# Performance work log

Measured on AMD Instinct MI355X. Metric: run time of the kernel, lower is better.

Reference implementation:

```python
import jax, jax.numpy as jnp
import numpy as np

B, T, D = 2, 2048, 1024
HEADS = 16
MEM = 512
HEAD_DIM = D // HEADS


def setup_inputs() -> dict:
    key = jax.random.key(0)
    k1, k2, k3, k4, k5 = jax.random.split(key, 5)
    x = jax.random.normal(k1, (B, T, D), dtype=jnp.float32)
    w_qkv = jax.random.normal(k2, (3 * D, D), dtype=jnp.float32) * (1.0 / np.sqrt(D))
    w_out = jax.random.normal(k3, (D, D), dtype=jnp.float32) * (1.0 / np.sqrt(D))
    b_out = jax.random.normal(k4, (D,), dtype=jnp.float32) * 0.01
    memory = jax.random.normal(k5, (MEM, D), dtype=jnp.float32)
    return {"x": x, "w_qkv": w_qkv, "w_out": w_out, "b_out": b_out, "memory": memory}


def reference(x, w_qkv, w_out, b_out, memory):
    b, t, d = x.shape
    h, hd = HEADS, HEAD_DIM
    scale = hd ** -0.5
    # QKV projection: [B,T,3D]
    qkv = jnp.einsum('btd,ed->bte', x, w_qkv)
    q, k, v = jnp.split(qkv, 3, axis=-1)
    # [B,H,T,hd]
    q = q.reshape(b, t, h, hd).transpose(0, 2, 1, 3)
    k = k.reshape(b, t, h, hd).transpose(0, 2, 1, 3)
    v = v.reshape(b, t, h, hd).transpose(0, 2, 1, 3)
    # memory K/V: [B,H,MEM,hd] (broadcast over batch)
    mem = memory.reshape(1, MEM, h, hd).transpose(0, 2, 1, 3)
    mem = jnp.broadcast_to(mem, (b, h, MEM, hd))
    k = jnp.concatenate([mem, k], axis=2)
    v = jnp.concatenate([mem, v], axis=2)
    # attention: scores [B,H,T,MEM+T]
    scores = jnp.einsum('bhqd,bhkd->bhqk', q, k) * scale
    weights = jax.nn.softmax(scores, axis=-1)
    out = jnp.einsum('bhqk,bhkd->bhqd', weights, v)
    out = out.transpose(0, 2, 1, 3).reshape(b, t, d)
    return jnp.einsum('btd,ed->bte', out, w_out) + b_out
```

## Files before the change

### kernel.cpp

```cpp
#include <hip/hip_runtime.h>
#include <hip/hip_bf16.h>
#include <stdint.h>

#define B_   2
#define T_   2048
#define D_   1024
#define H_   16
#define HD_  64
#define MEM_ 512
#define KV_  (MEM_ + T_)
#define NIT_ (KV_ / 64)

using bf16 = __bf16;
typedef __bf16 bf16x8 __attribute__((ext_vector_type(8)));
typedef float  f32x4  __attribute__((ext_vector_type(4)));
typedef short  s16x4  __attribute__((ext_vector_type(4)));

__device__ __forceinline__ f32x4 mfma16(bf16x8 a, bf16x8 b, f32x4 c) {
  return __builtin_amdgcn_mfma_f32_16x16x32_bf16(a, b, c, 0, 0, 0);
}
__device__ __forceinline__ f32x4 mfma16k16(s16x4 a, s16x4 b, f32x4 c) {
  return __builtin_amdgcn_mfma_f32_16x16x16bf16_1k(a, b, c, 0, 0, 0);
}

template <bool F32>
__device__ __forceinline__ bf16x8 load8(const void* p, size_t off) {
  if constexpr (F32) {
    const float* q = (const float*)p + off;
    f32x4 u = *(const f32x4*)q;
    f32x4 v = *(const f32x4*)(q + 4);
    bf16x8 r;
    r[0] = (bf16)u[0]; r[1] = (bf16)u[1]; r[2] = (bf16)u[2]; r[3] = (bf16)u[3];
    r[4] = (bf16)v[0]; r[5] = (bf16)v[1]; r[6] = (bf16)v[2]; r[7] = (bf16)v[3];
    return r;
  } else {
    return *(const bf16x8*)((const bf16*)p + off);
  }
}

__device__ __forceinline__ unsigned short bf16_bits(float f) {
  bf16 h = (bf16)f;
  return __builtin_bit_cast(unsigned short, h);
}

__device__ __forceinline__ ushort4 pack4(f32x4 v) {
  ushort4 p;
  p.x = bf16_bits(v[0]); p.y = bf16_bits(v[1]);
  p.z = bf16_bits(v[2]); p.w = bf16_bits(v[3]);
  return p;
}

__global__ void fill_mem(const float* __restrict__ memory,
                         bf16* __restrict__ mem_k, bf16* __restrict__ mem_vt) {
  int idx = blockIdx.x * 256 + threadIdx.x;
  int m = idx >> 10, d = idx & 1023;
  bf16 v = (bf16)memory[idx];
  mem_k[idx] = v;
  mem_vt[(size_t)d * MEM_ + m] = v;
}

template <int EPI, bool AF32, bool WF32, bool APLANE>
__global__ __launch_bounds__(256) void gemm_bt(
    const void* __restrict__ A, const void* __restrict__ W,
    const float* __restrict__ bias,
    bf16* __restrict__ q_ws, bf16* __restrict__ k_ws, bf16* __restrict__ vt_ws,
    float* __restrict__ Cout, int K) {
  __shared__ __align__(16) bf16 Als[128 * 32];
  __shared__ __align__(16) bf16 Bls[128 * 32];
  const int m0 = blockIdx.y * 128;
  const int n0 = blockIdx.x * 128;
  const int tid = threadIdx.x;
  const int w = tid >> 6;
  const int lane = tid & 63;
  const int lx = lane & 15;
  const int quad = lane >> 4;
  const int amb = (w & 1) * 64;
  const int bnb = (w >> 1) * 64;
  const int r0 = tid >> 2, seg = tid & 3;

  f32x4 acc[4][4];
#pragma unroll
  for (int i = 0; i < 4; i++)
#pragma unroll
    for (int j = 0; j < 4; j++) acc[i][j] = (f32x4){0.f, 0.f, 0.f, 0.f};

  for (int k0 = 0; k0 < K; k0 += 32) {
    bf16x8 a0, a1;
    if constexpr (APLANE) {
      int c0 = k0 + seg * 8, h = c0 >> 6, hd = c0 & 63;
      int mA = m0 + r0, mB = m0 + 64 + r0;
      a0 = load8<false>(A,
          ((size_t)((mA >> 11) * H_ + h) * T_ + (mA & 2047)) * HD_ + hd);
      a1 = load8<false>(A,
          ((size_t)((mB >> 11) * H_ + h) * T_ + (mB & 2047)) * HD_ + hd);
    } else {
      a0 = load8<AF32>(A, (size_t)(m0 + r0) * K + k0 + seg * 8);
      a1 = load8<AF32>(A, (size_t)(m0 + 64 + r0) * K + k0 + seg * 8);
    }
    bf16x8 b0 = load8<WF32>(W, (size_t)(n0 + r0) * K + k0 + seg * 8);
    bf16x8 b1 = load8<WF32>(W, (size_t)(n0 + 64 + r0) * K + k0 + seg * 8);
    __syncthreads();
    *(bf16x8*)&Als[tid * 8] = a0;
    *(bf16x8*)&Als[2048 + tid * 8] = a1;
    *(bf16x8*)&Bls[tid * 8] = b0;
    *(bf16x8*)&Bls[2048 + tid * 8] = b1;
    __syncthreads();

    bf16x8 af[4], bfr[4];
#pragma unroll
    for (int mt = 0; mt < 4; mt++)
      af[mt] = *(const bf16x8*)&Als[(amb + mt * 16 + lx) * 32 + quad * 8];
#pragma unroll
    for (int nt = 0; nt < 4; nt++)
      bfr[nt] = *(const bf16x8*)&Bls[(bnb + nt * 16 + lx) * 32 + quad * 8];
#pragma unroll
    for (int mt = 0; mt < 4; mt++)
#pragma unroll
      for (int nt = 0; nt < 4; nt++)
        acc[mt][nt] = mfma16(af[mt], bfr[nt], acc[mt][nt]);
  }

  if (EPI == 0) {
#pragma unroll
    for (int mt = 0; mt < 4; mt++) {
      int mbase = m0 + amb + mt * 16 + quad * 4;
      int b = mbase >> 11;
      int t = mbase & 2047;
#pragma unroll
      for (int nt = 0; nt < 4; nt++) {
        int col = n0 + bnb + nt * 16 + lx;
        int which = col >> 10;
        int d = col & 1023;
        int h = d >> 6, hdi = d & 63;
        int bh = b * H_ + h;
        if (which == 0) {
#pragma unroll
          for (int r = 0; r < 4; r++)
            q_ws[((size_t)bh * T_ + t + r) * HD_ + hdi] = (bf16)acc[mt][nt][r];
        } else if (which == 1) {
#pragma unroll
          for (int r = 0; r < 4; r++)
            k_ws[((size_t)bh * T_ + t + r) * HD_ + hdi] = (bf16)acc[mt][nt][r];
        } else {
          *(ushort4*)&vt_ws[((size_t)bh * HD_ + hdi) * T_ + t] =
              pack4(acc[mt][nt]);
        }
      }
    }
  } else {
#pragma unroll
    for (int nt = 0; nt < 4; nt++) {
      int col = n0 + bnb + nt * 16 + lx;
      float bias_f = bias[col];
#pragma unroll
      for (int mt = 0; mt < 4; mt++) {
        int mbase = m0 + amb + mt * 16 + quad * 4;
#pragma unroll
        for (int r = 0; r < 4; r++)
          Cout[(size_t)(mbase + r) * D_ + col] = acc[mt][nt][r] + bias_f;
      }
    }
  }
}

__global__ __launch_bounds__(256, 2) void attn_kernel(
    bf16* __restrict__ q_ws, const bf16* __restrict__ k_ws,
    const bf16* __restrict__ vt_ws, const bf16* __restrict__ mem_k,
    const bf16* __restrict__ mem_vt) {
  __shared__ __align__(16) bf16 Kls[64][72];
  __shared__ __align__(16) bf16 Vls[64][72];
  const int tid = threadIdx.x;
  const int w = tid >> 6;
  const int lane = tid & 63;
  const int lx = lane & 15;
  const int quad = lane >> 4;
  const int bh = blockIdx.x & 31;
  const int qt = blockIdx.x >> 5;
  const int q0 = qt * 128 + w * 32;
  const int h = bh & 15;

  const int srow1 = tid >> 3, soff1 = (tid & 7) * 8;
  const int srow2 = (tid + 256) >> 3, soff2 = soff1;

  bf16* qbase = q_ws + ((size_t)bh * T_ + q0) * HD_;

  const float QSCALE = 0.125f * 1.44269504089f;
  bf16x8 qf[2][2];
#pragma unroll
  for (int qg = 0; qg < 2; qg++)
#pragma unroll
    for (int hf = 0; hf < 2; hf++) {
      bf16x8 v = *(const bf16x8*)(qbase + (size_t)(qg * 16 + lx) * HD_ +
                                  hf * 32 + quad * 8);
#pragma unroll
      for (int i = 0; i < 8; i++)
        v[i] = (bf16)((float)v[i] * QSCALE);
      qf[qg][hf] = v;
    }

  const bf16* kplane = k_ws + (size_t)bh * T_ * HD_;
  const bf16* vtplane = vt_ws + (size_t)bh * HD_ * T_;
  const bf16* mkh = mem_k + h * HD_;
  const bf16* mvh = mem_vt + (size_t)h * HD_ * MEM_;

  f32x4 o[4][2];
#pragma unroll
  for (int mt = 0; mt < 4; mt++)
#pragma unroll
    for (int qg = 0; qg < 2; qg++) o[mt][qg] = (f32x4){0.f, 0.f, 0.f, 0.f};
  float lsum[2] = {0.f, 0.f};

  for (int it = 0; it < NIT_; it++) {
    const int kv0 = it * 64;
    const bool memPart = kv0 < MEM_;
    bf16x8 kr1, kr2, vr1, vr2;
    if (memPart) {
      kr1 = *(const bf16x8*)(mkh + (size_t)(kv0 + srow1) * D_ + soff1);
      kr2 = *(const bf16x8*)(mkh + (size_t)(kv0 + srow2) * D_ + soff2);
      vr1 = *(const bf16x8*)(mvh + (size_t)srow1 * MEM_ + kv0 + soff1);
      vr2 = *(const bf16x8*)(mvh + (size_t)srow2 * MEM_ + kv0 + soff2);
    } else {
      const int t0 = kv0 - MEM_;
      kr1 = *(const bf16x8*)(kplane + (size_t)(t0 + srow1) * HD_ + soff1);
      kr2 = *(const bf16x8*)(kplane + (size_t)(t0 + srow2) * HD_ + soff2);
      vr1 = *(const bf16x8*)(vtplane + (size_t)srow1 * T_ + t0 + soff1);
      vr2 = *(const bf16x8*)(vtplane + (size_t)srow2 * T_ + t0 + soff2);
    }
    __syncthreads();
    *(bf16x8*)&Kls[srow1][soff1] = kr1;
    *(bf16x8*)&Kls[srow2][soff2] = kr2;
    *(bf16x8*)&Vls[srow1][soff1] = vr1;
    *(bf16x8*)&Vls[srow2][soff2] = vr2;
    __syncthreads();

    f32x4 s[4][2];
#pragma unroll
    for (int g = 0; g < 4; g++) {
      bf16x8 ka0 = *(const bf16x8*)&Kls[g * 16 + lx][quad * 8];
      bf16x8 ka1 = *(const bf16x8*)&Kls[g * 16 + lx][32 + quad * 8];
#pragma unroll
      for (int qg = 0; qg < 2; qg++) {
        s[g][qg] = (f32x4){0.f, 0.f, 0.f, 0.f};
        s[g][qg] = mfma16(ka0, qf[qg][0], s[g][qg]);
        s[g][qg] = mfma16(ka1, qf[qg][1], s[g][qg]);
      }
    }

    s16x4 pb[2][4];
#pragma unroll
    for (int qg = 0; qg < 2; qg++) {
      float ps = 0.f;
#pragma unroll
      for (int g = 0; g < 4; g++) {
#pragma unroll
        for (int r = 0; r < 4; r++) {
          float p = __builtin_amdgcn_exp2f(s[g][qg][r]);
          ps += p;
          pb[qg][g][r] = (short)bf16_bits(p);
        }
      }
      lsum[qg] += ps;
    }

#pragma unroll
    for (int mt = 0; mt < 4; mt++) {
#pragma unroll
      for (int kk = 0; kk < 4; kk++) {
        s16x4 va = *(const s16x4*)&Vls[mt * 16 + lx][kk * 16 + quad * 4];
#pragma unroll
        for (int qg = 0; qg < 2; qg++)
          o[mt][qg] = mfma16k16(va, pb[qg][kk], o[mt][qg]);
      }
    }
  }

  float inv[2];
#pragma unroll
  for (int qg = 0; qg < 2; qg++) {
    float s2 = lsum[qg];
    s2 += __shfl_xor(s2, 16);
    s2 += __shfl_xor(s2, 32);
    inv[qg] = 1.f / s2;
  }

#pragma unroll
  for (int qg = 0; qg < 2; qg++) {
#pragma unroll
    for (int mt = 0; mt < 4; mt++) {
      f32x4 ov;
#pragma unroll
      for (int r = 0; r < 4; r++) ov[r] = o[mt][qg][r] * inv[qg];
      *(ushort4*)(qbase + (size_t)(qg * 16 + lx) * HD_ + mt * 16 + quad * 4)
          = pack4(ov);
    }
  }
}

extern "C" void kernel_launch(void* const* d_in, const int* in_sizes, int n_in,
                              void* d_out, int out_size, void* d_ws,
                              size_t ws_size, hipStream_t stream) {
  const void*  x      = d_in[0];
  const void*  w_qkv  = d_in[1];
  const void*  w_out  = d_in[2];
  const float* b_out  = (const float*)d_in[3];
  const float* memory = (const float*)d_in[4];

  char* ws = (char*)d_ws;
  bf16* q_ws   = (bf16*)(ws);
  bf16* k_ws   = (bf16*)(ws + (8u << 20));
  bf16* vt_ws  = (bf16*)(ws + (16u << 20));
  bf16* mem_k  = (bf16*)(ws + (24u << 20));
  bf16* mem_vt = (bf16*)(ws + (25u << 20));
  float* out = (float*)d_out;

  fill_mem<<<dim3(2048), dim3(256), 0, stream>>>(memory, mem_k, mem_vt);
  gemm_bt<0, true, true, false><<<dim3(24, 32), dim3(256), 0, stream>>>(
      x, w_qkv, nullptr, q_ws, k_ws, vt_ws, nullptr, 1024);
  attn_kernel<<<dim3(512), dim3(256), 0, stream>>>(
      q_ws, k_ws, vt_ws, mem_k, mem_vt);
  gemm_bt<1, false, true, true><<<dim3(8, 32), dim3(256), 0, stream>>>(
      q_ws, w_out, b_out, nullptr, nullptr, nullptr, out, 1024);
}
```

Measured before the change: 222.9 us.

## Fuse memory fill into QKV GEMM and double attention KV tile

Removes the separate fill_mem launch by adding an extra row of blocks to the QKV GEMM grid that converts memory to bf16 K and transposed V, reading with vectorised float4 loads. The attention kernel now stages 128 KV rows per iteration instead of 64, processing them in two halves, which halves the number of barrier pairs and global-load rounds. This costs more LDS per block, which may reduce occupancy. The fill blocks also run alongside GEMM blocks and keep scattered transposed stores.

```diff
diff --git a/kernel.cpp b/kernel.cpp
--- a/kernel.cpp
+++ b/kernel.cpp
@@ -9,7 +9,7 @@
 #define HD_  64
 #define MEM_ 512
 #define KV_  (MEM_ + T_)
-#define NIT_ (KV_ / 64)
+#define NIT2_ (KV_ / 128)
 
 using bf16 = __bf16;
 typedef __bf16 bf16x8 __attribute__((ext_vector_type(8)));
@@ -50,26 +50,35 @@
   return p;
 }
 
-__global__ void fill_mem(const float* __restrict__ memory,
-                         bf16* __restrict__ mem_k, bf16* __restrict__ mem_vt) {
-  int idx = blockIdx.x * 256 + threadIdx.x;
-  int m = idx >> 10, d = idx & 1023;
-  bf16 v = (bf16)memory[idx];
-  mem_k[idx] = v;
-  mem_vt[(size_t)d * MEM_ + m] = v;
-}
-
-template <int EPI, bool AF32, bool WF32, bool APLANE>
+template <int EPI, bool AF32, bool WF32, bool APLANE, bool FUSEFILL>
 __global__ __launch_bounds__(256) void gemm_bt(
     const void* __restrict__ A, const void* __restrict__ W,
     const float* __restrict__ bias,
     bf16* __restrict__ q_ws, bf16* __restrict__ k_ws, bf16* __restrict__ vt_ws,
-    float* __restrict__ Cout, int K) {
+    float* __restrict__ Cout, int K,
+    const float* __restrict__ memory, bf16* __restrict__ mem_k,
+    bf16* __restrict__ mem_vt) {
   __shared__ __align__(16) bf16 Als[128 * 32];
   __shared__ __align__(16) bf16 Bls[128 * 32];
+  const int tid = threadIdx.x;
+
+  if constexpr (FUSEFILL) {
+    if (blockIdx.y == 32) {
+      for (int i = blockIdx.x * 256 + tid; i < 131072; i += 24 * 256) {
+        size_t e = (size_t)i * 4;
+        f32x4 v = *(const f32x4*)(memory + e);
+        *(ushort4*)&mem_k[e] = pack4(v);
+        int m = (int)(e >> 10), d = (int)(e & 1023);
+#pragma unroll
+        for (int j = 0; j < 4; j++)
+          mem_vt[(size_t)(d + j) * MEM_ + m] = (bf16)v[j];
+      }
+      return;
+    }
+  }
+
   const int m0 = blockIdx.y * 128;
   const int n0 = blockIdx.x * 128;
-  const int tid = threadIdx.x;
   const int w = tid >> 6;
   const int lane = tid & 63;
   const int lx = lane & 15;
@@ -167,8 +176,8 @@
     bf16* __restrict__ q_ws, const bf16* __restrict__ k_ws,
     const bf16* __restrict__ vt_ws, const bf16* __restrict__ mem_k,
     const bf16* __restrict__ mem_vt) {
-  __shared__ __align__(16) bf16 Kls[64][72];
-  __shared__ __align__(16) bf16 Vls[64][72];
+  __shared__ __align__(16) bf16 Kls[128][72];
+  __shared__ __align__(16) bf16 Vls[64][136];
   const int tid = threadIdx.x;
   const int w = tid >> 6;
   const int lane = tid & 63;
@@ -179,8 +188,8 @@
   const int q0 = qt * 128 + w * 32;
   const int h = bh & 15;
 
-  const int srow1 = tid >> 3, soff1 = (tid & 7) * 8;
-  const int srow2 = (tid + 256) >> 3, soff2 = soff1;
+  const int srK = tid >> 3, scK = (tid & 7) * 8;
+  const int srV = tid >> 4, scV = (tid & 15) * 8;
 
   bf16* qbase = q_ws + ((size_t)bh * T_ + q0) * HD_;
 
@@ -210,66 +219,73 @@
     for (int qg = 0; qg < 2; qg++) o[mt][qg] = (f32x4){0.f, 0.f, 0.f, 0.f};
   float lsum[2] = {0.f, 0.f};
 
-  for (int it = 0; it < NIT_; it++) {
-    const int kv0 = it * 64;
+  for (int it = 0; it < NIT2_; it++) {
+    const int kv0 = it * 128;
     const bool memPart = kv0 < MEM_;
-    bf16x8 kr1, kr2, vr1, vr2;
+    bf16x8 kr[4], vr[4];
     if (memPart) {
-      kr1 = *(const bf16x8*)(mkh + (size_t)(kv0 + srow1) * D_ + soff1);
-      kr2 = *(const bf16x8*)(mkh + (size_t)(kv0 + srow2) * D_ + soff2);
-      vr1 = *(const bf16x8*)(mvh + (size_t)srow1 * MEM_ + kv0 + soff1);
-      vr2 = *(const bf16x8*)(mvh + (size_t)srow2 * MEM_ + kv0 + soff2);
+#pragma unroll
+      for (int j = 0; j < 4; j++) {
+        kr[j] = *(const bf16x8*)(mkh + (size_t)(kv0 + srK + 32 * j) * D_ + scK);
+        vr[j] = *(const bf16x8*)(mvh + (size_t)(srV + 16 * j) * MEM_ + kv0 + scV);
+      }
     } else {
       const int t0 = kv0 - MEM_;
-      kr1 = *(const bf16x8*)(kplane + (size_t)(t0 + srow1) * HD_ + soff1);
-      kr2 = *(const bf16x8*)(kplane + (size_t)(t0 + srow2) * HD_ + soff2);
-      vr1 = *(const bf16x8*)(vtplane + (size_t)srow1 * T_ + t0 + soff1);
-      vr2 = *(const bf16x8*)(vtplane + (size_t)srow2 * T_ + t0 + soff2);
+#pragma unroll
+      for (int j = 0; j < 4; j++) {
+        kr[j] = *(const bf16x8*)(kplane + (size_t)(t0 + srK + 32 * j) * HD_ + scK);
+        vr[j] = *(const bf16x8*)(vtplane + (size_t)(srV + 16 * j) * T_ + t0 + scV);
+      }
     }
     __syncthreads();
-    *(bf16x8*)&Kls[srow1][soff1] = kr1;
-    *(bf16x8*)&Kls[srow2][soff2] = kr2;
-    *(bf16x8*)&Vls[srow1][soff1] = vr1;
-    *(bf16x8*)&Vls[srow2][soff2] = vr2;
+#pragma unroll
+    for (int j = 0; j < 4; j++) {
+      *(bf16x8*)&Kls[srK + 32 * j][scK] = kr[j];
+      *(bf16x8*)&Vls[srV + 16 * j][scV] = vr[j];
+    }
     __syncthreads();
 
-    f32x4 s[4][2];
-#pragma unroll
-    for (int g = 0; g < 4; g++) {
-      bf16x8 ka0 = *(const bf16x8*)&Kls[g * 16 + lx][quad * 8];
-      bf16x8 ka1 = *(const bf16x8*)&Kls[g * 16 + lx][32 + quad * 8];
+#pragma unroll
+    for (int half = 0; half < 2; half++) {
+      const int ro = half * 64;
+      f32x4 s[4][2];
+#pragma unroll
+      for (int g = 0; g < 4; g++) {
+        bf16x8 ka0 = *(const bf16x8*)&Kls[ro + g * 16 + lx][quad * 8];
+        bf16x8 ka1 = *(const bf16x8*)&Kls[ro + g * 16 + lx][32 + quad * 8];
+#pragma unroll
+        for (int qg = 0; qg < 2; qg++) {
+          s[g][qg] = (f32x4){0.f, 0.f, 0.f, 0.f};
+          s[g][qg] = mfma16(ka0, qf[qg][0], s[g][qg]);
+          s[g][qg] = mfma16(ka1, qf[qg][1], s[g][qg]);
+        }
+      }
+
+      s16x4 pb[2][4];
 #pragma unroll
       for (int qg = 0; qg < 2; qg++) {
-        s[g][qg] = (f32x4){0.f, 0.f, 0.f, 0.f};
-        s[g][qg] = mfma16(ka0, qf[qg][0], s[g][qg]);
-        s[g][qg] = mfma16(ka1, qf[qg][1], s[g][qg]);
-      }
-    }
-
-    s16x4 pb[2][4];
-#pragma unroll
-    for (int qg = 0; qg < 2; qg++) {
-      float ps = 0.f;
-#pragma unroll
-      for (int g = 0; g < 4; g++) {
-#pragma unroll
-        for (int r = 0; r < 4; r++) {
-          float p = __builtin_amdgcn_exp2f(s[g][qg][r]);
-          ps += p;
-          pb[qg][g][r] = (short)bf16_bits(p);
+        float ps = 0.f;
+#pragma unroll
+        for (int g = 0; g < 4; g++) {
+#pragma unroll
+          for (int r = 0; r < 4; r++) {
+            float p = __builtin_amdgcn_exp2f(s[g][qg][r]);
+            ps += p;
+            pb[qg][g][r] = (short)bf16_bits(p);
+          }
         }
-      }
-      lsum[qg] += ps;
-    }
-
-#pragma unroll
-    for (int mt = 0; mt < 4; mt++) {
-#pragma unroll
-      for (int kk = 0; kk < 4; kk++) {
-        s16x4 va = *(const s16x4*)&Vls[mt * 16 + lx][kk * 16 + quad * 4];
-#pragma unroll
-        for (int qg = 0; qg < 2; qg++)
-          o[mt][qg] = mfma16k16(va, pb[qg][kk], o[mt][qg]);
+        lsum[qg] += ps;
+      }
+
+#pragma unroll
+      for (int mt = 0; mt < 4; mt++) {
+#pragma unroll
+        for (int kk = 0; kk < 4; kk++) {
+          s16x4 va = *(const s16x4*)&Vls[mt * 16 + lx][ro + kk * 16 + quad * 4];
+#pragma unroll
+          for (int qg = 0; qg < 2; qg++)
+            o[mt][qg] = mfma16k16(va, pb[qg][kk], o[mt][qg]);
+        }
       }
     }
   }
@@ -313,11 +329,12 @@
   bf16* mem_vt = (bf16*)(ws + (25u << 20));
   float* out = (float*)d_out;
 
-  fill_mem<<<dim3(2048), dim3(256), 0, stream>>>(memory, mem_k, mem_vt);
-  gemm_bt<0, true, true, false><<<dim3(24, 32), dim3(256), 0, stream>>>(
-      x, w_qkv, nullptr, q_ws, k_ws, vt_ws, nullptr, 1024);
+  gemm_bt<0, true, true, false, true><<<dim3(24, 33), dim3(256), 0, stream>>>(
+      x, w_qkv, nullptr, q_ws, k_ws, vt_ws, nullptr, 1024,
+      memory, mem_k, mem_vt);
   attn_kernel<<<dim3(512), dim3(256), 0, stream>>>(
       q_ws, k_ws, vt_ws, mem_k, mem_vt);
-  gemm_bt<1, false, true, true><<<dim3(8, 32), dim3(256), 0, stream>>>(
-      q_ws, w_out, b_out, nullptr, nullptr, nullptr, out, 1024);
-}
+  gemm_bt<1, false, true, true, false><<<dim3(8, 32), dim3(256), 0, stream>>>(
+      q_ws, w_out, b_out, nullptr, nullptr, nullptr, out, 1024,
+      nullptr, nullptr, nullptr);
+}
```

Result: slower. 232.4 us (+4.3%).
